# Performance work log

Hardware: AMD Instinct MI355X
Metric: run time of the kernel (lower is better)

## Reference

```python
import jax, jax.numpy as jnp
import numpy as np

B, HH, WW, C = 1, 96, 96, 128
HEADS, K = 4, 7

def setup_inputs() -> dict:
    key = jax.random.key(0)
    ks = jax.random.split(key, 6)
    def lin(k, o, i):
        return jax.random.normal(k, (o, i), jnp.float32) * (1.0 / np.sqrt(i))
    return {
        "x": jax.random.normal(ks[0], (B, HH, WW, C), jnp.float32),
        "qkv_w": lin(ks[1], 3 * C, C),
        "qkv_b": jnp.zeros((3 * C,), jnp.float32),
        "proj_w": lin(ks[2], C, C),
        "proj_b": jnp.zeros((C,), jnp.float32),
        "fc1_w": lin(ks[3], 4 * C, C),
        "fc1_b": jnp.zeros((4 * C,), jnp.float32),
        "fc2_w": lin(ks[4], C, 4 * C),
        "fc2_b": jnp.zeros((C,), jnp.float32),
    }

def _na2d(q, k, v):
    # q,k,v: [B, heads, H, W, hd]; NATTEN 2D neighborhood attention,
    # kernel K, stride 1, dilation 1, non-causal. Windows are clamped at
    # borders so each query attends to exactly K*K in-bounds keys.
    Bq, h, Hs, Ws, hd = q.shape
    start_h = jnp.clip(jnp.arange(Hs) - K // 2, 0, Hs - K)
    idx_h = start_h[:, None] + jnp.arange(K)  # [H, K]
    start_w = jnp.clip(jnp.arange(Ws) - K // 2, 0, Ws - K)
    idx_w = start_w[:, None] + jnp.arange(K)  # [W, K]
    I = idx_h[:, None, :, None]  # -> [H, W, K, K] broadcast
    J = idx_w[None, :, None, :]
    k_nb = k[:, :, I, J, :]  # [B, heads, H, W, K, K, hd]
    v_nb = v[:, :, I, J, :]
    scale = jnp.asarray(hd, q.dtype) ** -0.5
    logits = jnp.einsum('bhijd,bhijkld->bhijkl', q, k_nb) * scale
    attn = jax.nn.softmax(logits.reshape(Bq, h, Hs, Ws, K * K), axis=-1)
    attn = attn.reshape(Bq, h, Hs, Ws, K, K)
    return jnp.einsum('bhijkl,bhijkld->bhijd', attn, v_nb)

def reference(x, qkv_w, qkv_b, proj_w, proj_b, fc1_w, fc1_b, fc2_w, fc2_b):
    Bq, Hs, Ws, Cc = x.shape
    hd = Cc // HEADS
    qkv = x @ qkv_w.T + qkv_b  # [B,H,W,3C]
    q, k, v = jnp.split(qkv, 3, axis=-1)
    def to_heads(t):
        return t.reshape(Bq, Hs, Ws, HEADS, hd).transpose(0, 3, 1, 2, 4)
    o = _na2d(to_heads(q), to_heads(k), to_heads(v))  # [B,heads,H,W,hd]
    o = o.transpose(0, 2, 3, 1, 4).reshape(Bq, Hs, Ws, Cc)
    x0 = o @ proj_w.T + proj_b
    h1 = jax.nn.gelu(x0 @ fc1_w.T + fc1_b, approximate=False)
    return h1 @ fc2_w.T + fc2_b
```

## Files before the change

kernel.cpp:

```cpp
#include <hip/hip_runtime.h>

typedef __bf16 bf16_t;
typedef __bf16 bf16x8 __attribute__((ext_vector_type(8)));
typedef __bf16 bf16x4 __attribute__((ext_vector_type(4)));
typedef float f32x4 __attribute__((ext_vector_type(4)));

#define HH 96
#define WW 96
#define CC 128
#define HEADS 4
#define HD 32
#define TOK (HH * WW)
#define PLANE (TOK * CC)
#define KW 7

#define W_PROJ 0
#define W_FC1  16384
#define W_FC2  81920
#define W_TOT  147456

#define PATCH 10
#define PSZ 100
#define NPAD 112
#define STR 136
#define H1S 520

#define REGA_ELE ((NPAD + 16) * STR)
#define PBUF_ELE (4 * 16 * STR)
#define SMEM_BYTES ((REGA_ELE + PBUF_ELE) * 2)

__device__ __forceinline__ bf16x8 cvt8(const float* __restrict__ p) {
    const f32x4 a = *(const f32x4*)p;
    const f32x4 b = *(const f32x4*)(p + 4);
    bf16x8 r;
    r[0] = (bf16_t)a[0]; r[1] = (bf16_t)a[1]; r[2] = (bf16_t)a[2]; r[3] = (bf16_t)a[3];
    r[4] = (bf16_t)b[0]; r[5] = (bf16_t)b[1]; r[6] = (bf16_t)b[2]; r[7] = (bf16_t)b[3];
    return r;
}

template <int NT>
__device__ __forceinline__ void mmaN(const bf16_t* __restrict__ A, int lda,
                                     const bf16_t* __restrict__ W, int ldb,
                                     int K, f32x4* acc) {
    const int lane = threadIdx.x & 63;
    const bf16_t* ap = A + (lane & 15) * lda + ((lane >> 4) * 8);
    const bf16_t* bp = W + (lane & 15) * ldb + ((lane >> 4) * 8);
    for (int k0 = 0; k0 < K; k0 += 32) {
        bf16x8 a = *(const bf16x8*)(ap + k0);
#pragma unroll
        for (int t = 0; t < NT; t++) {
            bf16x8 b = *(const bf16x8*)(bp + t * 16 * ldb + k0);
            acc[t] = __builtin_amdgcn_mfma_f32_16x16x32_bf16(a, b, acc[t], 0, 0, 0);
        }
    }
}

__global__ __launch_bounds__(256) void k_qkv(const float* __restrict__ x,
                                             const float* __restrict__ qkv_w,
                                             const float* __restrict__ qkv_b,
                                             const float* __restrict__ proj_w,
                                             const float* __restrict__ fc1_w,
                                             const float* __restrict__ fc2_w,
                                             float* __restrict__ qf,
                                             bf16_t* __restrict__ kb,
                                             bf16_t* __restrict__ vb,
                                             bf16_t* __restrict__ wb) {
    const int tid = threadIdx.x, bid = blockIdx.x;
    {
        const int idx = bid * 256 + tid;
        if (idx < W_TOT / 4) {
            const int base = idx * 4;
            const float* src;
            if (base < W_FC1)      src = proj_w + base;
            else if (base < W_FC2) src = fc1_w + (base - W_FC1);
            else                   src = fc2_w + (base - W_FC2);
            const f32x4 a = *(const f32x4*)src;
            bf16x4 r;
            r[0] = (bf16_t)a[0]; r[1] = (bf16_t)a[1];
            r[2] = (bf16_t)a[2]; r[3] = (bf16_t)a[3];
            *(bf16x4*)(wb + base) = r;
        }
    }
    const int w = tid >> 6, lane = tid & 63;
    const int g = lane >> 4, li = lane & 15;
    const int m0 = bid * 16;
    const float* ap = x + (m0 + li) * CC + g * 8;
    const float* bp = qkv_w + (w * 96 + li) * CC + g * 8;
    f32x4 acc[6] = {};
    for (int k0 = 0; k0 < CC; k0 += 32) {
        bf16x8 a = cvt8(ap + k0);
#pragma unroll
        for (int t = 0; t < 6; t++) {
            bf16x8 b = cvt8(bp + t * 16 * CC + k0);
            acc[t] = __builtin_amdgcn_mfma_f32_16x16x32_bf16(a, b, acc[t], 0, 0, 0);
        }
    }
#pragma unroll
    for (int t = 0; t < 6; t++) {
        const int n = w * 96 + t * 16 + li;
        const float bb = qkv_b[n];
        const int part = n >> 7, c = n & 127;
#pragma unroll
        for (int r = 0; r < 4; r++) {
            const int m = m0 + g * 4 + r;
            const float val = acc[t][r] + bb;
            if (part == 0)      qf[m * CC + c] = val;
            else if (part == 1) kb[m * CC + c] = (bf16_t)val;
            else                vb[m * CC + c] = (bf16_t)val;
        }
    }
}

__global__ __launch_bounds__(256, 3) void k_attn_mlp(
        float* __restrict__ qof,
        const bf16_t* __restrict__ kg,
        const bf16_t* __restrict__ vg,
        const bf16_t* __restrict__ wb,
        const float* __restrict__ proj_b,
        const float* __restrict__ fc1_b,
        const float* __restrict__ fc2_b) {
    __shared__ __align__(16) bf16_t smem[REGA_ELE + PBUF_ELE];
    bf16_t* ks   = smem;
    bf16_t* qs   = smem + NPAD * STR;
    bf16_t* vst  = smem;
    bf16_t* h1s  = smem;
    bf16_t* Pbuf = smem + REGA_ELE;
    bf16_t* o_s  = Pbuf;
    bf16_t* x0s  = Pbuf + 16 * STR;

    const int tid = threadIdx.x;
    const int w = tid >> 6, lane = tid & 63;
    const int g = lane >> 4, li = lane & 15;
    const int bid = blockIdx.x;
    const int bi = bid / 24, bj = bid % 24;
    const int i0 = bi * 4, j0 = bj * 4;
    const int pr0 = min(max(i0 - 3, 0), HH - PATCH);
    const int pc0 = min(max(j0 - 3, 0), WW - PATCH);
    const int head = w;

    for (int idx = tid; idx < PSZ * 16; idx += 256) {
        const int row = idx >> 4, c8 = idx & 15;
        const int pi = row / PATCH, pj = row - PATCH * pi;
        *(bf16x8*)(ks + row * STR + c8 * 8) =
            *(const bf16x8*)(kg + ((pr0 + pi) * WW + (pc0 + pj)) * CC + c8 * 8);
    }
    {
        const int row = tid >> 4, c8 = tid & 15;
        const int ti = row >> 2, tj = row & 3;
        *(bf16x8*)(qs + row * STR + c8 * 8) =
            cvt8(qof + ((i0 + ti) * WW + (j0 + tj)) * CC + c8 * 8);
    }
    __syncthreads();

    f32x4 lg[7];
    {
        const bf16x8 aq = *(const bf16x8*)(qs + li * STR + head * HD + g * 8);
#pragma unroll
        for (int t = 0; t < 7; t++) {
            const bf16x8 bk = *(const bf16x8*)(ks + (t * 16 + li) * STR + head * HD + g * 8);
            lg[t] = __builtin_amdgcn_mfma_f32_16x16x32_bf16(aq, bk, (f32x4){0.f,0.f,0.f,0.f}, 0, 0, 0);
        }
    }
    int lr[4], lc[4];
#pragma unroll
    for (int r = 0; r < 4; r++) {
        const int m = g * 4 + r;
        const int i = i0 + (m >> 2), j = j0 + (m & 3);
        lr[r] = min(max(i - 3, 0), HH - KW) - pr0;
        lc[r] = min(max(j - 3, 0), WW - KW) - pc0;
    }
    const float scale = 0.17677669529663687f;
#pragma unroll
    for (int t = 0; t < 7; t++) {
        const int col = t * 16 + li;
        const int pi = col / PATCH, pj = col - PATCH * pi;
#pragma unroll
        for (int r = 0; r < 4; r++) {
            const bool valid = (col < PSZ) &&
                               ((unsigned)(pi - lr[r]) <= 6u) &&
                               ((unsigned)(pj - lc[r]) <= 6u);
            lg[t][r] = valid ? lg[t][r] * scale : -1e30f;
        }
    }
    f32x4 mx = lg[0], sm;
#pragma unroll
    for (int t = 1; t < 7; t++)
#pragma unroll
        for (int r = 0; r < 4; r++) mx[r] = fmaxf(mx[r], lg[t][r]);
#pragma unroll
    for (int off = 8; off; off >>= 1)
#pragma unroll
        for (int r = 0; r < 4; r++) mx[r] = fmaxf(mx[r], __shfl_xor(mx[r], off));
#pragma unroll
    for (int r = 0; r < 4; r++) sm[r] = 0.f;
#pragma unroll
    for (int t = 0; t < 7; t++)
#pragma unroll
        for (int r = 0; r < 4; r++) {
            lg[t][r] = __expf(lg[t][r] - mx[r]);
            sm[r] += lg[t][r];
        }
#pragma unroll
    for (int off = 8; off; off >>= 1)
#pragma unroll
        for (int r = 0; r < 4; r++) sm[r] += __shfl_xor(sm[r], off);
#pragma unroll
    for (int r = 0; r < 4; r++) sm[r] = 1.f / sm[r];

    bf16_t* Pw = Pbuf + w * 16 * STR;
#pragma unroll
    for (int t = 0; t < 7; t++)
#pragma unroll
        for (int r = 0; r < 4; r++)
            Pw[(g * 4 + r) * STR + t * 16 + li] = (bf16_t)(lg[t][r] * sm[r]);
    *(bf16x4*)(Pw + (lane >> 2) * STR + NPAD + (lane & 3) * 4) = (bf16x4){0,0,0,0};
    __syncthreads();

    for (int idx = tid; idx < PSZ * 16; idx += 256) {
        const int c8 = idx / PSZ, p = idx - c8 * PSZ;
        const int pi = p / PATCH, pj = p - PATCH * pi;
        const bf16x8 t = *(const bf16x8*)(vg + ((pr0 + pi) * WW + (pc0 + pj)) * CC + c8 * 8);
#pragma unroll
        for (int e = 0; e < 8; e++) vst[(c8 * 8 + e) * STR + p] = t[e];
    }
    for (int idx = tid; idx < 128 * 8; idx += 256) {
        const int row = idx >> 3, c4 = idx & 7;
        *(bf16x4*)(vst + row * STR + PSZ + c4 * 4) = (bf16x4){0,0,0,0};
    }
    __syncthreads();

    f32x4 oA[2] = {};
#pragma unroll
    for (int ks0 = 0; ks0 < 128; ks0 += 32) {
        const bf16x8 a = *(const bf16x8*)(Pw + li * STR + ks0 + g * 8);
#pragma unroll
        for (int t2 = 0; t2 < 2; t2++) {
            const bf16x8 b = *(const bf16x8*)(vst + (head * HD + t2 * 16 + li) * STR + ks0 + g * 8);
            oA[t2] = __builtin_amdgcn_mfma_f32_16x16x32_bf16(a, b, oA[t2], 0, 0, 0);
        }
    }
    __syncthreads();

#pragma unroll
    for (int t2 = 0; t2 < 2; t2++)
#pragma unroll
        for (int r = 0; r < 4; r++)
            o_s[(g * 4 + r) * STR + head * HD + t2 * 16 + li] = (bf16_t)oA[t2][r];
    __syncthreads();

    {
        f32x4 acc[2] = {};
        mmaN<2>(o_s, STR, wb + W_PROJ + (w * 32) * CC, CC, CC, acc);
#pragma unroll
        for (int t = 0; t < 2; t++) {
            const int n = w * 32 + t * 16 + li;
            const float bb = proj_b[n];
#pragma unroll
            for (int r = 0; r < 4; r++)
                x0s[(g * 4 + r) * STR + n] = (bf16_t)(acc[t][r] + bb);
        }
    }
    __syncthreads();

    {
        f32x4 acc[8] = {};
        mmaN<8>(x0s, STR, wb + W_FC1 + (w * 128) * CC, CC, CC, acc);
#pragma unroll
        for (int t = 0; t < 8; t++) {
            const int n = w * 128 + t * 16 + li;
            const float bb = fc1_b[n];
#pragma unroll
            for (int r = 0; r < 4; r++) {
                const int m = g * 4 + r;
                const float xv = acc[t][r] + bb;
                const float u = 0.7978845608028654f * (xv + 0.044715f * xv * xv * xv);
                const float e = __expf(2.f * u);
                const float gg = 0.5f * xv * (2.f - 2.f / (e + 1.f));
                h1s[m * H1S + n] = (bf16_t)gg;
            }
        }
    }
    __syncthreads();

    {
        f32x4 acc[2] = {};
        mmaN<2>(h1s, H1S, wb + W_FC2 + (w * 32) * (4 * CC), 4 * CC, 4 * CC, acc);
#pragma unroll
        for (int t = 0; t < 2; t++) {
            const int n = w * 32 + t * 16 + li;
            const float bb = fc2_b[n];
#pragma unroll
            for (int r = 0; r < 4; r++) {
                const int m = g * 4 + r;
                const int i = i0 + (m >> 2), j = j0 + (m & 3);
                float xv = acc[t][r] + bb;
                xv = fminf(fmaxf(xv, -1e4f), 1e4f);
                qof[(i * WW + j) * CC + n] = xv;
            }
        }
    }
}

extern "C" void kernel_launch(void* const* d_in, const int* in_sizes, int n_in,
                              void* d_out, int out_size, void* d_ws, size_t ws_size,
                              hipStream_t stream) {
    const float* x      = (const float*)d_in[0];
    const float* qkv_w  = (const float*)d_in[1];
    const float* qkv_b  = (const float*)d_in[2];
    const float* proj_w = (const float*)d_in[3];
    const float* proj_b = (const float*)d_in[4];
    const float* fc1_w  = (const float*)d_in[5];
    const float* fc1_b  = (const float*)d_in[6];
    const float* fc2_w  = (const float*)d_in[7];
    const float* fc2_b  = (const float*)d_in[8];

    float* qof = (float*)d_out;
    bf16_t* ws = (bf16_t*)d_ws;
    bf16_t* kb = ws;
    bf16_t* vb = ws + PLANE;
    bf16_t* wb = ws + 2 * PLANE;

    k_qkv     <<<576, 256, 0, stream>>>(x, qkv_w, qkv_b, proj_w, fc1_w, fc2_w,
                                        qof, kb, vb, wb);
    k_attn_mlp<<<576, 256, 0, stream>>>(qof, kb, vb, wb, proj_b, fc1_b, fc2_b);
}
```

Measured before the change: 129.3 us.

## Fuse QKV projection into attention block, recomputing K/V over halo patch

Drops the separate QKV kernel that wrote Q (fp32), K and V (bf16) to global memory. Each attention block now computes the QKV projection itself for its 10x10 halo patch and writes K, transposed V and the 16 interior Q rows straight into shared memory. Weight conversion moves to a small separate kernel. This removes the global round trip for q/k/v, at the cost of recomputing the projection for overlapping halo tokens (about 100/16 redundancy), reading fp32 qkv_w on every block, and a larger shared-memory footprint with occupancy hint lowered to 2.

```diff
diff --git a/kernel.cpp b/kernel.cpp
--- a/kernel.cpp
+++ b/kernel.cpp
@@ -8,10 +8,7 @@
 #define HH 96
 #define WW 96
 #define CC 128
-#define HEADS 4
 #define HD 32
-#define TOK (HH * WW)
-#define PLANE (TOK * CC)
 #define KW 7
 
 #define W_PROJ 0
@@ -25,9 +22,10 @@
 #define STR 136
 #define H1S 520
 
-#define REGA_ELE ((NPAD + 16) * STR)
-#define PBUF_ELE (4 * 16 * STR)
-#define SMEM_BYTES ((REGA_ELE + PBUF_ELE) * 2)
+#define R0 0
+#define R1 (NPAD * STR)
+#define R2 (R1 + 128 * STR)
+#define SME (R2 + 16 * STR)
 
 __device__ __forceinline__ bf16x8 cvt8(const float* __restrict__ p) {
     const f32x4 a = *(const f32x4*)p;
@@ -55,100 +53,96 @@
     }
 }
 
-__global__ __launch_bounds__(256) void k_qkv(const float* __restrict__ x,
-                                             const float* __restrict__ qkv_w,
-                                             const float* __restrict__ qkv_b,
-                                             const float* __restrict__ proj_w,
+__global__ __launch_bounds__(256) void k_cvt(const float* __restrict__ proj_w,
                                              const float* __restrict__ fc1_w,
                                              const float* __restrict__ fc2_w,
-                                             float* __restrict__ qf,
-                                             bf16_t* __restrict__ kb,
-                                             bf16_t* __restrict__ vb,
                                              bf16_t* __restrict__ wb) {
-    const int tid = threadIdx.x, bid = blockIdx.x;
-    {
-        const int idx = bid * 256 + tid;
-        if (idx < W_TOT / 4) {
-            const int base = idx * 4;
-            const float* src;
-            if (base < W_FC1)      src = proj_w + base;
-            else if (base < W_FC2) src = fc1_w + (base - W_FC1);
-            else                   src = fc2_w + (base - W_FC2);
-            const f32x4 a = *(const f32x4*)src;
-            bf16x4 r;
-            r[0] = (bf16_t)a[0]; r[1] = (bf16_t)a[1];
-            r[2] = (bf16_t)a[2]; r[3] = (bf16_t)a[3];
-            *(bf16x4*)(wb + base) = r;
-        }
-    }
-    const int w = tid >> 6, lane = tid & 63;
-    const int g = lane >> 4, li = lane & 15;
-    const int m0 = bid * 16;
-    const float* ap = x + (m0 + li) * CC + g * 8;
-    const float* bp = qkv_w + (w * 96 + li) * CC + g * 8;
-    f32x4 acc[6] = {};
-    for (int k0 = 0; k0 < CC; k0 += 32) {
-        bf16x8 a = cvt8(ap + k0);
-#pragma unroll
-        for (int t = 0; t < 6; t++) {
-            bf16x8 b = cvt8(bp + t * 16 * CC + k0);
-            acc[t] = __builtin_amdgcn_mfma_f32_16x16x32_bf16(a, b, acc[t], 0, 0, 0);
-        }
-    }
-#pragma unroll
-    for (int t = 0; t < 6; t++) {
-        const int n = w * 96 + t * 16 + li;
-        const float bb = qkv_b[n];
-        const int part = n >> 7, c = n & 127;
-#pragma unroll
-        for (int r = 0; r < 4; r++) {
-            const int m = m0 + g * 4 + r;
-            const float val = acc[t][r] + bb;
-            if (part == 0)      qf[m * CC + c] = val;
-            else if (part == 1) kb[m * CC + c] = (bf16_t)val;
-            else                vb[m * CC + c] = (bf16_t)val;
-        }
-    }
-}
-
-__global__ __launch_bounds__(256, 3) void k_attn_mlp(
-        float* __restrict__ qof,
-        const bf16_t* __restrict__ kg,
-        const bf16_t* __restrict__ vg,
+    const int idx = blockIdx.x * 256 + threadIdx.x;
+    const int base = idx * 4;
+    const float* src;
+    if (base < W_FC1)      src = proj_w + base;
+    else if (base < W_FC2) src = fc1_w + (base - W_FC1);
+    else                   src = fc2_w + (base - W_FC2);
+    const f32x4 a = *(const f32x4*)src;
+    bf16x4 r;
+    r[0] = (bf16_t)a[0]; r[1] = (bf16_t)a[1]; r[2] = (bf16_t)a[2]; r[3] = (bf16_t)a[3];
+    *(bf16x4*)(wb + base) = r;
+}
+
+__global__ __launch_bounds__(256, 2) void k_block(
+        const float* __restrict__ x,
+        const float* __restrict__ qkv_w, const float* __restrict__ qkv_b,
         const bf16_t* __restrict__ wb,
-        const float* __restrict__ proj_b,
-        const float* __restrict__ fc1_b,
-        const float* __restrict__ fc2_b) {
-    __shared__ __align__(16) bf16_t smem[REGA_ELE + PBUF_ELE];
-    bf16_t* ks   = smem;
-    bf16_t* qs   = smem + NPAD * STR;
-    bf16_t* vst  = smem;
-    bf16_t* h1s  = smem;
-    bf16_t* Pbuf = smem + REGA_ELE;
-    bf16_t* o_s  = Pbuf;
-    bf16_t* x0s  = Pbuf + 16 * STR;
+        const float* __restrict__ proj_b, const float* __restrict__ fc1_b,
+        const float* __restrict__ fc2_b,  float* __restrict__ out) {
+    __shared__ __align__(16) bf16_t smem[SME];
+    bf16_t* ks   = smem + R0;
+    bf16_t* vt   = smem + R1;
+    bf16_t* qs   = smem + R2;
+    bf16_t* Pbuf = smem + R0;
+    bf16_t* o_s  = smem + R2;
+    bf16_t* x0s  = smem + R0;
+    bf16_t* h1s  = smem + R0 + 16 * STR;
 
     const int tid = threadIdx.x;
     const int w = tid >> 6, lane = tid & 63;
     const int g = lane >> 4, li = lane & 15;
     const int bid = blockIdx.x;
-    const int bi = bid / 24, bj = bid % 24;
-    const int i0 = bi * 4, j0 = bj * 4;
+    const int i0 = (bid / 24) * 4, j0 = (bid % 24) * 4;
     const int pr0 = min(max(i0 - 3, 0), HH - PATCH);
     const int pc0 = min(max(j0 - 3, 0), WW - PATCH);
+    const int oa = i0 - pr0, ob = j0 - pc0;
     const int head = w;
 
-    for (int idx = tid; idx < PSZ * 16; idx += 256) {
-        const int row = idx >> 4, c8 = idx & 15;
-        const int pi = row / PATCH, pj = row - PATCH * pi;
-        *(bf16x8*)(ks + row * STR + c8 * 8) =
-            *(const bf16x8*)(kg + ((pr0 + pi) * WW + (pc0 + pj)) * CC + c8 * 8);
-    }
-    {
-        const int row = tid >> 4, c8 = tid & 15;
-        const int ti = row >> 2, tj = row & 3;
-        *(bf16x8*)(qs + row * STR + c8 * 8) =
-            cvt8(qof + ((i0 + ti) * WW + (j0 + tj)) * CC + c8 * 8);
+    {
+        const int row = tid >> 1, half = tid & 1;
+        *(bf16x8*)(vt + row * STR + NPAD + half * 8) = (bf16x8){0,0,0,0,0,0,0,0};
+    }
+
+    float bb6[6];
+#pragma unroll
+    for (int nt = 0; nt < 6; nt++) bb6[nt] = qkv_b[w * 96 + nt * 16 + li];
+
+    for (int mt = 0; mt < 7; mt++) {
+        const int arow = mt * 16 + li;
+        const int r99 = min(arow, 99);
+        const int pi = r99 / 10, pj = r99 - 10 * pi;
+        const float* ax = x + ((pr0 + pi) * WW + (pc0 + pj)) * CC + g * 8;
+        bf16x8 a[4];
+#pragma unroll
+        for (int k0 = 0; k0 < 4; k0++) a[k0] = cvt8(ax + k0 * 32);
+#pragma unroll
+        for (int nt = 0; nt < 6; nt++) {
+            const int n = w * 96 + nt * 16 + li;
+            const float* bp = qkv_w + n * CC + g * 8;
+            f32x4 acc = {0.f, 0.f, 0.f, 0.f};
+#pragma unroll
+            for (int k0 = 0; k0 < 4; k0++)
+                acc = __builtin_amdgcn_mfma_f32_16x16x32_bf16(a[k0], cvt8(bp + k0 * 32), acc, 0, 0, 0);
+            const float bb = bb6[nt];
+            const int part = n >> 7, c = n & 127;
+            if (part == 0) {
+#pragma unroll
+                for (int r = 0; r < 4; r++) {
+                    const int row = mt * 16 + g * 4 + r;
+                    if (row < PSZ) {
+                        const int ppi = row / 10, ppj = row - 10 * ppi;
+                        const int ta = ppi - oa, tb = ppj - ob;
+                        if ((unsigned)ta < 4u && (unsigned)tb < 4u)
+                            qs[(ta * 4 + tb) * STR + c] = (bf16_t)(acc[r] + bb);
+                    }
+                }
+            } else if (part == 1) {
+#pragma unroll
+                for (int r = 0; r < 4; r++)
+                    ks[(mt * 16 + g * 4 + r) * STR + c] = (bf16_t)(acc[r] + bb);
+            } else {
+                bf16x4 pk;
+#pragma unroll
+                for (int r = 0; r < 4; r++) pk[r] = (bf16_t)(acc[r] + bb);
+                *(bf16x4*)(vt + c * STR + mt * 16 + g * 4) = pk;
+            }
+        }
     }
     __syncthreads();
 
@@ -173,7 +167,7 @@
 #pragma unroll
     for (int t = 0; t < 7; t++) {
         const int col = t * 16 + li;
-        const int pi = col / PATCH, pj = col - PATCH * pi;
+        const int pi = col / 10, pj = col - 10 * pi;
 #pragma unroll
         for (int r = 0; r < 4; r++) {
             const bool valid = (col < PSZ) &&
@@ -207,6 +201,8 @@
 #pragma unroll
     for (int r = 0; r < 4; r++) sm[r] = 1.f / sm[r];
 
+    __syncthreads();
+
     bf16_t* Pw = Pbuf + w * 16 * STR;
 #pragma unroll
     for (int t = 0; t < 7; t++)
@@ -216,26 +212,13 @@
     *(bf16x4*)(Pw + (lane >> 2) * STR + NPAD + (lane & 3) * 4) = (bf16x4){0,0,0,0};
     __syncthreads();
 
-    for (int idx = tid; idx < PSZ * 16; idx += 256) {
-        const int c8 = idx / PSZ, p = idx - c8 * PSZ;
-        const int pi = p / PATCH, pj = p - PATCH * pi;
-        const bf16x8 t = *(const bf16x8*)(vg + ((pr0 + pi) * WW + (pc0 + pj)) * CC + c8 * 8);
-#pragma unroll
-        for (int e = 0; e < 8; e++) vst[(c8 * 8 + e) * STR + p] = t[e];
-    }
-    for (int idx = tid; idx < 128 * 8; idx += 256) {
-        const int row = idx >> 3, c4 = idx & 7;
-        *(bf16x4*)(vst + row * STR + PSZ + c4 * 4) = (bf16x4){0,0,0,0};
-    }
-    __syncthreads();
-
     f32x4 oA[2] = {};
 #pragma unroll
     for (int ks0 = 0; ks0 < 128; ks0 += 32) {
         const bf16x8 a = *(const bf16x8*)(Pw + li * STR + ks0 + g * 8);
 #pragma unroll
         for (int t2 = 0; t2 < 2; t2++) {
-            const bf16x8 b = *(const bf16x8*)(vst + (head * HD + t2 * 16 + li) * STR + ks0 + g * 8);
+            const bf16x8 b = *(const bf16x8*)(vt + (head * HD + t2 * 16 + li) * STR + ks0 + g * 8);
             oA[t2] = __builtin_amdgcn_mfma_f32_16x16x32_bf16(a, b, oA[t2], 0, 0, 0);
         }
     }
@@ -295,7 +278,7 @@
                 const int i = i0 + (m >> 2), j = j0 + (m & 3);
                 float xv = acc[t][r] + bb;
                 xv = fminf(fmaxf(xv, -1e4f), 1e4f);
-                qof[(i * WW + j) * CC + n] = xv;
+                out[(i * WW + j) * CC + n] = xv;
             }
         }
     }
@@ -314,13 +297,10 @@
     const float* fc2_w  = (const float*)d_in[7];
     const float* fc2_b  = (const float*)d_in[8];
 
-    float* qof = (float*)d_out;
-    bf16_t* ws = (bf16_t*)d_ws;
-    bf16_t* kb = ws;
-    bf16_t* vb = ws + PLANE;
-    bf16_t* wb = ws + 2 * PLANE;
-
-    k_qkv     <<<576, 256, 0, stream>>>(x, qkv_w, qkv_b, proj_w, fc1_w, fc2_w,
-                                        qof, kb, vb, wb);
-    k_attn_mlp<<<576, 256, 0, stream>>>(qof, kb, vb, wb, proj_b, fc1_b, fc2_b);
-}
+    bf16_t* wb = (bf16_t*)d_ws;
+    float* out = (float*)d_out;
+
+    k_cvt  <<<144, 256, 0, stream>>>(proj_w, fc1_w, fc2_w, wb);
+    k_block<<<576, 256, 0, stream>>>(x, qkv_w, qkv_b, wb,
+                                     proj_b, fc1_b, fc2_b, out);
+}
```

Measured after the change: 147.3 us. 1.14x slower.
